# Kernel optimization log

Hardware: AMD Instinct MI355X
Metric: run time of the kernel (lower is better)

Reference implementation:

```python
import jax, jax.numpy as jnp
import numpy as np
from jax import lax

SOS_IDX = 1
EOS_IDX = 2

B, T, K = 32, 256, 128


def setup_inputs() -> dict:
    key = jax.random.key(0)
    k1, k2, k3, k4 = jax.random.split(key, 4)
    h = jax.random.normal(k1, (B, T, K), dtype=jnp.float32)
    transition = jax.random.normal(k2, (K, K), dtype=jnp.float32) * 0.1
    y = jax.random.randint(k3, (B, T), 0, K)
    lengths = jnp.maximum(jax.random.randint(k4, (B,), 1, T + 1), 1)
    mask = jnp.arange(T)[None, :] < lengths[:, None]  # [B, T] bool, contiguous prefix
    return {"h": h, "transition": transition, "y": y, "lengths": lengths, "mask": mask}


def reference(h, transition, y, lengths, mask):
    """CRF negative log-likelihood, same math as CRF.nll."""
    b, t_len, k = h.shape
    # crf_scores[b,t,i,j] = h[b,t,j] + transition[i,j]
    scores = h[:, :, None, :] + transition[None, None, :, :]  # [B,T,K,K]

    # Golden path score: score of transition prev_tag -> tag at each valid step.
    prev_y = jnp.concatenate(
        [jnp.full((b, 1), SOS_IDX, dtype=y.dtype), y[:, :-1]], axis=1
    )  # [B,T]
    gold = jnp.take_along_axis(
        jnp.take_along_axis(scores, prev_y[:, :, None, None], axis=2)[:, :, 0, :],
        y[:, :, None],
        axis=2,
    )[:, :, 0]  # [B,T]
    golden_scores = jnp.sum(jnp.where(mask, gold, jnp.zeros((), h.dtype)))

    # Forward (alpha) recurrence in log space; freeze alpha past sequence end.
    alpha0 = scores[:, 0, SOS_IDX, :]  # [B,K] (all lengths >= 1)
    scores_tbkk = jnp.swapaxes(scores, 0, 1)  # [T,B,K,K]
    mask_tb = jnp.swapaxes(mask, 0, 1)  # [T,B]

    def step(alpha, xs):
        s_t, m_t = xs  # [B,K,K], [B]
        new_alpha = jax.nn.logsumexp(s_t + alpha[:, :, None], axis=1)  # [B,K]
        return jnp.where(m_t[:, None], new_alpha, alpha), None

    alpha, _ = lax.scan(step, alpha0, (scores_tbkk[1:], mask_tb[1:]))
    Z = jnp.sum(alpha[:, EOS_IDX])
    loss = (Z - golden_scores) / b
    return loss
```

## Files before the change

kernel.cpp:

```cpp
#include <hip/hip_runtime.h>
#include <stdint.h>

#define SOS_IDX 1
#define EOS_IDX 2
#define Bb 32
#define Tt 256
#define Kk 128
#define SK 136
#define CSP 16

typedef unsigned short ushort_t;
typedef __attribute__((ext_vector_type(8))) short short8;
typedef __attribute__((ext_vector_type(4))) float float4v;

__device__ __forceinline__ ushort_t f2bf(float x) {
    union { float f; uint32_t u; } c; c.f = x;
    uint32_t u = c.u + 0x7FFFu + ((c.u >> 16) & 1u);
    return (ushort_t)(u >> 16);
}
__device__ __forceinline__ float bf2f(ushort_t s) {
    union { uint32_t u; float f; } c; c.u = ((uint32_t)s) << 16;
    return c.f;
}
__device__ __forceinline__ float bflo(uint32_t u) {
    union { uint32_t u; float f; } c; c.u = u << 16; return c.f;
}
__device__ __forceinline__ float bfhi(uint32_t u) {
    union { uint32_t u; float f; } c; c.u = u & 0xFFFF0000u; return c.f;
}
__device__ __forceinline__ uint32_t pk2bf(float a, float b) {
    union { float f; uint32_t u; } ca, cb; ca.f = a; cb.f = b;
    uint32_t ua = ca.u + 0x7FFFu + ((ca.u >> 16) & 1u);
    uint32_t ub = cb.u + 0x7FFFu + ((cb.u >> 16) & 1u);
    return __builtin_amdgcn_perm(ub, ua, 0x07060302u);
}

__global__ __launch_bounds__(256) void crf_prep(const float* __restrict__ trans,
                                                ushort_t* __restrict__ ETT,
                                                ushort_t* __restrict__ ET) {
    const int tid = threadIdx.x, bid = blockIdx.x;
    int idx = ((bid & 7) * 256 + tid) * 8;
    if (bid < 8) {
        int m = idx >> 7, k0 = idx & 127;
        float e[8];
#pragma unroll
        for (int r = 0; r < 8; ++r) e[r] = __expf(trans[(k0 + r) * Kk + m]);
        uint4 o;
        o.x = pk2bf(e[0], e[1]); o.y = pk2bf(e[2], e[3]);
        o.z = pk2bf(e[4], e[5]); o.w = pk2bf(e[6], e[7]);
        *(uint4*)&ETT[idx] = o;
    } else {
        float4 a = *(const float4*)&trans[idx];
        float4 b = *(const float4*)&trans[idx + 4];
        uint4 o;
        o.x = pk2bf(__expf(a.x), __expf(a.y));
        o.y = pk2bf(__expf(a.z), __expf(a.w));
        o.z = pk2bf(__expf(b.x), __expf(b.y));
        o.w = pk2bf(__expf(b.z), __expf(b.w));
        *(uint4*)&ET[idx] = o;
    }
}

__global__ __launch_bounds__(128, 2) void crf_stageA(const float* __restrict__ h,
                                                     const ushort_t* __restrict__ ETT,
                                                     const ushort_t* __restrict__ ET,
                                                     const int* __restrict__ lengths,
                                                     ushort_t* __restrict__ Qt,
                                                     float* __restrict__ Ls,
                                                     int NC) {
    const int st = blockIdx.x, b = blockIdx.y, c = blockIdx.z;
    const int tid = threadIdx.x;
    const int lane = tid & 63, w = tid >> 6;
    const int c15 = lane & 15, q = lane >> 4;
    const int len = lengths[b];
    int ts = c * CSP; if (ts < 1) ts = 1;
    int te = (c + 1) * CSP; if (te > Tt) te = Tt;
    const int tE = te < len ? te : len;
    if (ts >= tE) return;
    const int nsteps = tE - ts;
    const size_t qoff = ((size_t)b * NC + c) * (Kk * Kk);
    const int nbase = st * 32;

    __shared__ __align__(16) ushort_t s_S[2][32 * SK];
    __shared__ __align__(16) float    s_eh[CSP][Kk];
    __shared__ float s_wmax[2][2];

    for (int tl = w; tl < nsteps; tl += 2) {
        const float* hr = &h[((size_t)b * Tt + ts + tl) * Kk];
        s_eh[tl][lane]      = __expf(hr[lane]);
        s_eh[tl][lane + 64] = __expf(hr[lane + 64]);
    }

    short8 afr[4][4];
#pragma unroll
    for (int mt = 0; mt < 4; ++mt)
#pragma unroll
        for (int kt = 0; kt < 4; ++kt)
            afr[mt][kt] = *(const short8*)&ETT[(w * 64 + mt * 16 + c15) * Kk + kt * 32 + q * 8];
    __syncthreads();

    {
        float lmax = 0.0f;
#pragma unroll
        for (int j = 0; j < 4; ++j) {
            int idx = j * 128 + tid;
            int nl = idx >> 4, k8 = (idx & 15) * 8;
            uint4 ev = *(const uint4*)&ET[(nbase + nl) * Kk + k8];
            float4 e0 = *(const float4*)&s_eh[0][k8];
            float4 e1 = *(const float4*)&s_eh[0][k8 + 4];
            float v0 = bflo(ev.x) * e0.x, v1 = bfhi(ev.x) * e0.y;
            float v2 = bflo(ev.y) * e0.z, v3 = bfhi(ev.y) * e0.w;
            float v4 = bflo(ev.z) * e1.x, v5 = bfhi(ev.z) * e1.y;
            float v6 = bflo(ev.w) * e1.z, v7 = bfhi(ev.w) * e1.w;
            lmax = fmaxf(lmax, fmaxf(fmaxf(fmaxf(v0, v1), fmaxf(v2, v3)),
                                     fmaxf(fmaxf(v4, v5), fmaxf(v6, v7))));
            uint4 o;
            o.x = pk2bf(v0, v1); o.y = pk2bf(v2, v3);
            o.z = pk2bf(v4, v5); o.w = pk2bf(v6, v7);
            *(uint4*)&s_S[0][nl * SK + k8] = o;
        }
#pragma unroll
        for (int o = 1; o < 64; o <<= 1) lmax = fmaxf(lmax, __shfl_xor(lmax, o));
        if (lane == 0) s_wmax[0][w] = lmax;
    }
    __syncthreads();

    float L = 0.0f;
    int cur = 0;
    for (int s = 1; s < nsteps; ++s) {
        float invG = 1.0f;
        if ((s & 3) == 0) {
            int ms = ((s >> 2) - 1) & 1;
            float g = fmaxf(s_wmax[ms][0], s_wmax[ms][1]);
            invG = 1.0f / g;
            L += __logf(g);
        }
        const bool isMark = ((s & 3) == 3) || (s == nsteps - 1);

        float sc[4][4];
#pragma unroll
        for (int mt = 0; mt < 4; ++mt) {
            float4 e = *(const float4*)&s_eh[s][w * 64 + mt * 16 + q * 4];
            sc[mt][0] = e.x * invG; sc[mt][1] = e.y * invG;
            sc[mt][2] = e.z * invG; sc[mt][3] = e.w * invG;
        }

        short8 bfr[2][4];
        const ushort_t* ps = s_S[cur];
#pragma unroll
        for (int nt = 0; nt < 2; ++nt)
#pragma unroll
            for (int kt = 0; kt < 4; ++kt)
                bfr[nt][kt] = *(const short8*)&ps[(nt * 16 + c15) * SK + kt * 32 + q * 8];

        float4v acc[4][2];
#pragma unroll
        for (int mt = 0; mt < 4; ++mt)
#pragma unroll
            for (int nt = 0; nt < 2; ++nt) acc[mt][nt] = (float4v){0.f, 0.f, 0.f, 0.f};
#pragma unroll
        for (int kt = 0; kt < 4; ++kt)
#pragma unroll
            for (int mt = 0; mt < 4; ++mt)
#pragma unroll
                for (int nt = 0; nt < 2; ++nt)
                    acc[mt][nt] = __builtin_amdgcn_mfma_f32_16x16x32_bf16(
                        afr[mt][kt], bfr[nt][kt], acc[mt][nt], 0, 0, 0);

        int nxt = cur ^ 1;
        ushort_t* pn = s_S[nxt];
        float lmax = 0.0f;
#pragma unroll
        for (int mt = 0; mt < 4; ++mt)
#pragma unroll
            for (int nt = 0; nt < 2; ++nt) {
                float v0 = acc[mt][nt][0] * sc[mt][0];
                float v1 = acc[mt][nt][1] * sc[mt][1];
                float v2 = acc[mt][nt][2] * sc[mt][2];
                float v3 = acc[mt][nt][3] * sc[mt][3];
                if (isMark)
                    lmax = fmaxf(lmax, fmaxf(fmaxf(v0, v1), fmaxf(v2, v3)));
                uint2 u; u.x = pk2bf(v0, v1); u.y = pk2bf(v2, v3);
                *(uint2*)&pn[(nt * 16 + c15) * SK + w * 64 + mt * 16 + q * 4] = u;
            }
        if (isMark) {
#pragma unroll
            for (int o = 1; o < 64; o <<= 1) lmax = fmaxf(lmax, __shfl_xor(lmax, o));
            if (lane == 0) s_wmax[(s >> 2) & 1][w] = lmax;
        }
        __syncthreads();
        cur = nxt;
    }

    int fs = ((nsteps - 1) >> 2) & 1;
    float Gf = fmaxf(s_wmax[fs][0], s_wmax[fs][1]);
    float dsc = 1.0f / Gf;
    L += __logf(Gf);
    const ushort_t* pc = s_S[cur];
#pragma unroll
    for (int j = 0; j < 4; ++j) {
        int idx = j * 128 + tid;
        int n = idx & 127, o = idx >> 7;
        uint4 gv; ushort_t* gp = (ushort_t*)&gv;
#pragma unroll
        for (int r = 0; r < 8; ++r)
            gp[r] = f2bf(bf2f(pc[(o * 8 + r) * SK + n]) * dsc);
        *(uint4*)&Qt[qoff + (size_t)n * Kk + nbase + o * 8] = gv;
    }
    if (tid == 0) Ls[(((size_t)b * NC + c) << 2) + st] = L;
}

__global__ __launch_bounds__(512, 1) void crf_stageB(const float* __restrict__ h,
                                                     const float* __restrict__ trans,
                                                     const int* __restrict__ y,
                                                     const int* __restrict__ lengths,
                                                     const ushort_t* __restrict__ Qt,
                                                     const float* __restrict__ Ls,
                                                     float* __restrict__ out,
                                                     int NC) {
    const int b = blockIdx.x;
    const int tid = threadIdx.x;
    const int lane = tid & 63, w = tid >> 6;
    const int n = tid >> 2, qr = tid & 3;
    const int len = lengths[b];

    __shared__ __align__(16) float vbuf[2][Kk];
    __shared__ float s_wmax[2][8];
    __shared__ float red[8];
    __shared__ float gred[4];

    if (w < 4) {
        float g = 0.0f;
        if (tid < len) {
            int yt   = y[b * Tt + tid];
            int prev = (tid == 0) ? SOS_IDX : y[b * Tt + tid - 1];
            g = h[((size_t)b * Tt + tid) * Kk + yt] + trans[prev * Kk + yt];
        }
#pragma unroll
        for (int off = 32; off > 0; off >>= 1) g += __shfl_down(g, off);
        if (lane == 0) gred[w] = g;
    }

    float a0 = h[((size_t)b * Tt) * Kk + n] + trans[SOS_IDX * Kk + n];
    float m0 = a0;
#pragma unroll
    for (int o = 1; o < 64; o <<= 1) m0 = fmaxf(m0, __shfl_xor(m0, o));
    if (lane == 0) red[w] = m0;
    __syncthreads();
    {
        float4 r0 = *(const float4*)&red[0];
        float4 r1 = *(const float4*)&red[4];
        m0 = fmaxf(fmaxf(fmaxf(r0.x, r0.y), fmaxf(r0.z, r0.w)),
                   fmaxf(fmaxf(r1.x, r1.y), fmaxf(r1.z, r1.w)));
    }
    float cacc = m0;
    if (qr == 0) vbuf[0][n] = __expf(a0 - m0);

    const int NCR = (len <= 1) ? 0 : min(NC, (len + CSP - 1) / CSP);
    const size_t lbase = (size_t)b * NC;
    uint4 qb[4];
    if (NCR > 0) {
        const uint4* qp = (const uint4*)(Qt + lbase * (Kk * Kk) + n * Kk + qr * 32);
#pragma unroll
        for (int r = 0; r < 4; ++r) qb[r] = qp[r];
    }
    __syncthreads();
    if (tid == 0)
        atomicAdd(out, -(gred[0] + gred[1] + gred[2] + gred[3]) * (1.0f / (float)Bb));

    int cur = 0;
    for (int ci = 0; ci < NCR; ++ci) {
        uint4 qn[4];
        if (ci + 1 < NCR) {
            const uint4* qp2 = (const uint4*)(Qt + (lbase + ci + 1) * (Kk * Kk) + n * Kk + qr * 32);
#pragma unroll
            for (int r = 0; r < 4; ++r) qn[r] = qp2[r];
        }
        float4 Ls4 = *(const float4*)&Ls[(lbase + ci) << 2];
        float Lref = fmaxf(fmaxf(Ls4.x, Ls4.y), fmaxf(Ls4.z, Ls4.w));
        float lsq = (qr == 0) ? Ls4.x : (qr == 1) ? Ls4.y : (qr == 2) ? Ls4.z : Ls4.w;
        float eQ = __expf(lsq - Lref);
        float invG = 1.0f;
        if (ci > 0 && (ci & 3) == 0) {
            int ms = ((ci >> 2) - 1) & 1;
            float4 r0 = *(const float4*)&s_wmax[ms][0];
            float4 r1 = *(const float4*)&s_wmax[ms][4];
            float g = fmaxf(fmaxf(fmaxf(r0.x, r0.y), fmaxf(r0.z, r0.w)),
                            fmaxf(fmaxf(r1.x, r1.y), fmaxf(r1.z, r1.w)));
            invG = 1.0f / g;
            cacc += __logf(g);
        }
        cacc += Lref;

        float acc0 = 0.0f, acc1 = 0.0f;
#pragma unroll
        for (int r = 0; r < 4; ++r) {
            uint4 d = qb[r];
            float4 v0 = *(const float4*)&vbuf[cur][qr * 32 + r * 8];
            float4 v1 = *(const float4*)&vbuf[cur][qr * 32 + r * 8 + 4];
            acc0 = fmaf(bflo(d.x), v0.x, acc0);
            acc1 = fmaf(bfhi(d.x), v0.y, acc1);
            acc0 = fmaf(bflo(d.y), v0.z, acc0);
            acc1 = fmaf(bfhi(d.y), v0.w, acc1);
            acc0 = fmaf(bflo(d.z), v1.x, acc0);
            acc1 = fmaf(bfhi(d.z), v1.y, acc1);
            acc0 = fmaf(bflo(d.w), v1.z, acc0);
            acc1 = fmaf(bfhi(d.w), v1.w, acc1);
        }
        float s = (acc0 + acc1) * (eQ * invG);
        s += __shfl_xor(s, 1);
        s += __shfl_xor(s, 2);

        const bool isMark = ((ci & 3) == 3) || (ci == NCR - 1);
        if (isMark) {
            float wm = s;
#pragma unroll
            for (int o = 1; o < 64; o <<= 1) wm = fmaxf(wm, __shfl_xor(wm, o));
            if (lane == 0) s_wmax[(ci >> 2) & 1][w] = wm;
        }
        int nxt = cur ^ 1;
        if (qr == 0) vbuf[nxt][n] = s;
        __syncthreads();
        cur = nxt;
        if (ci + 1 < NCR) {
#pragma unroll
            for (int r = 0; r < 4; ++r) qb[r] = qn[r];
        }
    }

    if (tid == 0) {
        atomicAdd(out, (cacc + __logf(vbuf[cur][EOS_IDX])) * (1.0f / (float)Bb));
    }
}

extern "C" void kernel_launch(void* const* d_in, const int* in_sizes, int n_in,
                              void* d_out, int out_size, void* d_ws, size_t ws_size,
                              hipStream_t stream) {
    const float* h       = (const float*)d_in[0];
    const float* trans   = (const float*)d_in[1];
    const int*   y       = (const int*)d_in[2];
    const int*   lengths = (const int*)d_in[3];
    float* out = (float*)d_out;

    const int NC = Tt / CSP;
    ushort_t* Qt  = (ushort_t*)d_ws;
    ushort_t* ETT = Qt + (size_t)Bb * NC * Kk * Kk;
    ushort_t* ET  = ETT + Kk * Kk;
    float*    Ls  = (float*)(ET + Kk * Kk);

    hipMemsetAsync(out, 0, sizeof(float), stream);
    crf_prep<<<16, 256, 0, stream>>>(trans, ETT, ET);
    crf_stageA<<<dim3(4, Bb, NC), 128, 0, stream>>>(h, ETT, ET, lengths, Qt, Ls, NC);
    crf_stageB<<<Bb, 512, 0, stream>>>(h, trans, y, lengths, Qt, Ls, out, NC);
}
```

Baseline: 112.8 us.

## Fuse prep, chunk-product and combine stages into one kernel with last-block combine

Merges the three kernels into one. Each block now computes exp(transition) to bf16 directly instead of reading a precomputed table. The per-batch serial combine runs in whichever block finishes last, detected with an atomic counter per batch and threadfences. This removes two launches and the launch gaps between stages, but adds redundant exp work in every block, an extra memset, and a serial combine done by only 128 threads with no prefetch of the next Qt chunk.

```diff
diff --git a/kernel.cpp b/kernel.cpp
--- a/kernel.cpp
+++ b/kernel.cpp
@@ -8,6 +8,7 @@
 #define Kk 128
 #define SK 136
 #define CSP 16
+#define NCc 16
 
 typedef unsigned short ushort_t;
 typedef __attribute__((ext_vector_type(8))) short short8;
@@ -35,55 +36,44 @@
     return __builtin_amdgcn_perm(ub, ua, 0x07060302u);
 }
 
-__global__ __launch_bounds__(256) void crf_prep(const float* __restrict__ trans,
-                                                ushort_t* __restrict__ ETT,
-                                                ushort_t* __restrict__ ET) {
-    const int tid = threadIdx.x, bid = blockIdx.x;
-    int idx = ((bid & 7) * 256 + tid) * 8;
-    if (bid < 8) {
-        int m = idx >> 7, k0 = idx & 127;
-        float e[8];
-#pragma unroll
-        for (int r = 0; r < 8; ++r) e[r] = __expf(trans[(k0 + r) * Kk + m]);
-        uint4 o;
-        o.x = pk2bf(e[0], e[1]); o.y = pk2bf(e[2], e[3]);
-        o.z = pk2bf(e[4], e[5]); o.w = pk2bf(e[6], e[7]);
-        *(uint4*)&ETT[idx] = o;
-    } else {
-        float4 a = *(const float4*)&trans[idx];
-        float4 b = *(const float4*)&trans[idx + 4];
-        uint4 o;
-        o.x = pk2bf(__expf(a.x), __expf(a.y));
-        o.y = pk2bf(__expf(a.z), __expf(a.w));
-        o.z = pk2bf(__expf(b.x), __expf(b.y));
-        o.w = pk2bf(__expf(b.z), __expf(b.w));
-        *(uint4*)&ET[idx] = o;
-    }
-}
-
-__global__ __launch_bounds__(128, 2) void crf_stageA(const float* __restrict__ h,
-                                                     const ushort_t* __restrict__ ETT,
-                                                     const ushort_t* __restrict__ ET,
-                                                     const int* __restrict__ lengths,
-                                                     ushort_t* __restrict__ Qt,
-                                                     float* __restrict__ Ls,
-                                                     int NC) {
+__global__ __launch_bounds__(128, 2) void crf_fused(const float* __restrict__ h,
+                                                    const float* __restrict__ trans,
+                                                    const int* __restrict__ y,
+                                                    const int* __restrict__ lengths,
+                                                    ushort_t* __restrict__ Qt,
+                                                    float* __restrict__ Ls,
+                                                    unsigned* __restrict__ cnt,
+                                                    float* __restrict__ out) {
     const int st = blockIdx.x, b = blockIdx.y, c = blockIdx.z;
     const int tid = threadIdx.x;
     const int lane = tid & 63, w = tid >> 6;
     const int c15 = lane & 15, q = lane >> 4;
     const int len = lengths[b];
+    const int NCRb = (len <= 1) ? 0 : ((len + CSP - 1) / CSP);
     int ts = c * CSP; if (ts < 1) ts = 1;
     int te = (c + 1) * CSP; if (te > Tt) te = Tt;
     const int tE = te < len ? te : len;
-    if (ts >= tE) return;
-    const int nsteps = tE - ts;
-    const size_t qoff = ((size_t)b * NC + c) * (Kk * Kk);
-    const int nbase = st * 32;
 
     __shared__ __align__(16) ushort_t s_S[2][32 * SK];
     __shared__ __align__(16) float    s_eh[CSP][Kk];
     __shared__ float s_wmax[2][2];
+    __shared__ __align__(16) float vbuf[2][Kk];
+    __shared__ float s_wm[2][2];
+    __shared__ float red2[2], gred2[2];
+    __shared__ unsigned s_last;
+
+    if (ts >= tE) {
+        if (st == 0 && c == 0 && tid == 0) {
+            int y0 = y[b * Tt];
+            float gold0 = h[(size_t)b * Tt * Kk + y0] + trans[SOS_IDX * Kk + y0];
+            float zb = h[(size_t)b * Tt * Kk + EOS_IDX] + trans[SOS_IDX * Kk + EOS_IDX];
+            atomicAdd(out, (zb - gold0) * (1.0f / (float)Bb));
+        }
+        return;
+    }
+    const int nsteps = tE - ts;
+    const size_t qoff = ((size_t)b * NCc + c) * (Kk * Kk);
+    const int nbase = st * 32;
 
     for (int tl = w; tl < nsteps; tl += 2) {
         const float* hr = &h[((size_t)b * Tt + ts + tl) * Kk];
@@ -95,8 +85,16 @@
 #pragma unroll
     for (int mt = 0; mt < 4; ++mt)
 #pragma unroll
-        for (int kt = 0; kt < 4; ++kt)
-            afr[mt][kt] = *(const short8*)&ETT[(w * 64 + mt * 16 + c15) * Kk + kt * 32 + q * 8];
+        for (int kt = 0; kt < 4; ++kt) {
+            short8 f;
+            int m = w * 64 + mt * 16 + c15;
+#pragma unroll
+            for (int j = 0; j < 8; ++j) {
+                int k = kt * 32 + q * 8 + j;
+                f[j] = (short)f2bf(__expf(trans[k * Kk + m]));
+            }
+            afr[mt][kt] = f;
+        }
     __syncthreads();
 
     {
@@ -105,13 +103,13 @@
         for (int j = 0; j < 4; ++j) {
             int idx = j * 128 + tid;
             int nl = idx >> 4, k8 = (idx & 15) * 8;
-            uint4 ev = *(const uint4*)&ET[(nbase + nl) * Kk + k8];
+            const float* tr = &trans[(nbase + nl) * Kk + k8];
             float4 e0 = *(const float4*)&s_eh[0][k8];
             float4 e1 = *(const float4*)&s_eh[0][k8 + 4];
-            float v0 = bflo(ev.x) * e0.x, v1 = bfhi(ev.x) * e0.y;
-            float v2 = bflo(ev.y) * e0.z, v3 = bfhi(ev.y) * e0.w;
-            float v4 = bflo(ev.z) * e1.x, v5 = bfhi(ev.z) * e1.y;
-            float v6 = bflo(ev.w) * e1.z, v7 = bfhi(ev.w) * e1.w;
+            float v0 = __expf(tr[0]) * e0.x, v1 = __expf(tr[1]) * e0.y;
+            float v2 = __expf(tr[2]) * e0.z, v3 = __expf(tr[3]) * e0.w;
+            float v4 = __expf(tr[4]) * e1.x, v5 = __expf(tr[5]) * e1.y;
+            float v6 = __expf(tr[6]) * e1.z, v7 = __expf(tr[7]) * e1.w;
             lmax = fmaxf(lmax, fmaxf(fmaxf(fmaxf(v0, v1), fmaxf(v2, v3)),
                                      fmaxf(fmaxf(v4, v5), fmaxf(v6, v7))));
             uint4 o;
@@ -207,129 +205,100 @@
             gp[r] = f2bf(bf2f(pc[(o * 8 + r) * SK + n]) * dsc);
         *(uint4*)&Qt[qoff + (size_t)n * Kk + nbase + o * 8] = gv;
     }
-    if (tid == 0) Ls[(((size_t)b * NC + c) << 2) + st] = L;
-}
-
-__global__ __launch_bounds__(512, 1) void crf_stageB(const float* __restrict__ h,
-                                                     const float* __restrict__ trans,
-                                                     const int* __restrict__ y,
-                                                     const int* __restrict__ lengths,
-                                                     const ushort_t* __restrict__ Qt,
-                                                     const float* __restrict__ Ls,
-                                                     float* __restrict__ out,
-                                                     int NC) {
-    const int b = blockIdx.x;
-    const int tid = threadIdx.x;
-    const int lane = tid & 63, w = tid >> 6;
-    const int n = tid >> 2, qr = tid & 3;
-    const int len = lengths[b];
-
-    __shared__ __align__(16) float vbuf[2][Kk];
-    __shared__ float s_wmax[2][8];
-    __shared__ float red[8];
-    __shared__ float gred[4];
-
-    if (w < 4) {
+    if (tid == 0) Ls[(((size_t)b * NCc + c) << 2) + st] = L;
+
+    __threadfence();
+    __syncthreads();
+    if (tid == 0) {
+        unsigned old = atomicAdd(&cnt[b], 1u);
+        s_last = (old == (unsigned)(4 * NCRb) - 1u) ? 1u : 0u;
+    }
+    __syncthreads();
+    if (!s_last) return;
+    __threadfence();
+
+    {
         float g = 0.0f;
         if (tid < len) {
             int yt   = y[b * Tt + tid];
             int prev = (tid == 0) ? SOS_IDX : y[b * Tt + tid - 1];
             g = h[((size_t)b * Tt + tid) * Kk + yt] + trans[prev * Kk + yt];
         }
+        int t1 = tid + 128;
+        if (t1 < len) {
+            int yt   = y[b * Tt + t1];
+            int prev = y[b * Tt + t1 - 1];
+            g += h[((size_t)b * Tt + t1) * Kk + yt] + trans[prev * Kk + yt];
+        }
 #pragma unroll
         for (int off = 32; off > 0; off >>= 1) g += __shfl_down(g, off);
-        if (lane == 0) gred[w] = g;
-    }
-
-    float a0 = h[((size_t)b * Tt) * Kk + n] + trans[SOS_IDX * Kk + n];
+        if (lane == 0) gred2[w] = g;
+    }
+
+    float a0 = h[((size_t)b * Tt) * Kk + tid] + trans[SOS_IDX * Kk + tid];
     float m0 = a0;
 #pragma unroll
     for (int o = 1; o < 64; o <<= 1) m0 = fmaxf(m0, __shfl_xor(m0, o));
-    if (lane == 0) red[w] = m0;
-    __syncthreads();
-    {
-        float4 r0 = *(const float4*)&red[0];
-        float4 r1 = *(const float4*)&red[4];
-        m0 = fmaxf(fmaxf(fmaxf(r0.x, r0.y), fmaxf(r0.z, r0.w)),
-                   fmaxf(fmaxf(r1.x, r1.y), fmaxf(r1.z, r1.w)));
-    }
+    if (lane == 0) red2[w] = m0;
+    __syncthreads();
+    m0 = fmaxf(red2[0], red2[1]);
     float cacc = m0;
-    if (qr == 0) vbuf[0][n] = __expf(a0 - m0);
-
-    const int NCR = (len <= 1) ? 0 : min(NC, (len + CSP - 1) / CSP);
-    const size_t lbase = (size_t)b * NC;
-    uint4 qb[4];
-    if (NCR > 0) {
-        const uint4* qp = (const uint4*)(Qt + lbase * (Kk * Kk) + n * Kk + qr * 32);
-#pragma unroll
-        for (int r = 0; r < 4; ++r) qb[r] = qp[r];
-    }
-    __syncthreads();
-    if (tid == 0)
-        atomicAdd(out, -(gred[0] + gred[1] + gred[2] + gred[3]) * (1.0f / (float)Bb));
-
-    int cur = 0;
-    for (int ci = 0; ci < NCR; ++ci) {
-        uint4 qn[4];
-        if (ci + 1 < NCR) {
-            const uint4* qp2 = (const uint4*)(Qt + (lbase + ci + 1) * (Kk * Kk) + n * Kk + qr * 32);
-#pragma unroll
-            for (int r = 0; r < 4; ++r) qn[r] = qp2[r];
-        }
+    vbuf[0][tid] = __expf(a0 - m0);
+    __syncthreads();
+
+    const size_t lbase = (size_t)b * NCc;
+    int cb = 0;
+    for (int ci = 0; ci < NCRb; ++ci) {
         float4 Ls4 = *(const float4*)&Ls[(lbase + ci) << 2];
         float Lref = fmaxf(fmaxf(Ls4.x, Ls4.y), fmaxf(Ls4.z, Ls4.w));
-        float lsq = (qr == 0) ? Ls4.x : (qr == 1) ? Ls4.y : (qr == 2) ? Ls4.z : Ls4.w;
-        float eQ = __expf(lsq - Lref);
+        float e0 = __expf(Ls4.x - Lref), e1 = __expf(Ls4.y - Lref);
+        float e2 = __expf(Ls4.z - Lref), e3 = __expf(Ls4.w - Lref);
         float invG = 1.0f;
         if (ci > 0 && (ci & 3) == 0) {
             int ms = ((ci >> 2) - 1) & 1;
-            float4 r0 = *(const float4*)&s_wmax[ms][0];
-            float4 r1 = *(const float4*)&s_wmax[ms][4];
-            float g = fmaxf(fmaxf(fmaxf(r0.x, r0.y), fmaxf(r0.z, r0.w)),
-                            fmaxf(fmaxf(r1.x, r1.y), fmaxf(r1.z, r1.w)));
-            invG = 1.0f / g;
-            cacc += __logf(g);
+            float gg = fmaxf(s_wm[ms][0], s_wm[ms][1]);
+            invG = 1.0f / gg;
+            cacc += __logf(gg);
         }
         cacc += Lref;
 
-        float acc0 = 0.0f, acc1 = 0.0f;
-#pragma unroll
-        for (int r = 0; r < 4; ++r) {
-            uint4 d = qb[r];
-            float4 v0 = *(const float4*)&vbuf[cur][qr * 32 + r * 8];
-            float4 v1 = *(const float4*)&vbuf[cur][qr * 32 + r * 8 + 4];
-            acc0 = fmaf(bflo(d.x), v0.x, acc0);
-            acc1 = fmaf(bfhi(d.x), v0.y, acc1);
-            acc0 = fmaf(bflo(d.y), v0.z, acc0);
-            acc1 = fmaf(bfhi(d.y), v0.w, acc1);
-            acc0 = fmaf(bflo(d.z), v1.x, acc0);
-            acc1 = fmaf(bfhi(d.z), v1.y, acc1);
-            acc0 = fmaf(bflo(d.w), v1.z, acc0);
-            acc1 = fmaf(bfhi(d.w), v1.w, acc1);
-        }
-        float s = (acc0 + acc1) * (eQ * invG);
-        s += __shfl_xor(s, 1);
-        s += __shfl_xor(s, 2);
-
-        const bool isMark = ((ci & 3) == 3) || (ci == NCR - 1);
+        const uint4* qp = (const uint4*)(Qt + (lbase + ci) * (Kk * Kk) + (size_t)tid * Kk);
+        float p0 = 0.f, p1 = 0.f, p2 = 0.f, p3 = 0.f;
+#pragma unroll
+        for (int r = 0; r < 16; ++r) {
+            uint4 d = qp[r];
+            float4 v0 = *(const float4*)&vbuf[cb][r * 8];
+            float4 v1 = *(const float4*)&vbuf[cb][r * 8 + 4];
+            float* pp = (r < 4) ? &p0 : (r < 8) ? &p1 : (r < 12) ? &p2 : &p3;
+            float a = *pp;
+            a = fmaf(bflo(d.x), v0.x, a);
+            a = fmaf(bfhi(d.x), v0.y, a);
+            a = fmaf(bflo(d.y), v0.z, a);
+            a = fmaf(bfhi(d.y), v0.w, a);
+            a = fmaf(bflo(d.z), v1.x, a);
+            a = fmaf(bfhi(d.z), v1.y, a);
+            a = fmaf(bflo(d.w), v1.z, a);
+            a = fmaf(bfhi(d.w), v1.w, a);
+            *pp = a;
+        }
+        float s = (fmaf(e0, p0, e1 * p1) + fmaf(e2, p2, e3 * p3)) * invG;
+
+        const bool isMark = ((ci & 3) == 3) || (ci == NCRb - 1);
         if (isMark) {
             float wm = s;
 #pragma unroll
             for (int o = 1; o < 64; o <<= 1) wm = fmaxf(wm, __shfl_xor(wm, o));
-            if (lane == 0) s_wmax[(ci >> 2) & 1][w] = wm;
-        }
-        int nxt = cur ^ 1;
-        if (qr == 0) vbuf[nxt][n] = s;
+            if (lane == 0) s_wm[(ci >> 2) & 1][w] = wm;
+        }
+        int nxt = cb ^ 1;
+        vbuf[nxt][tid] = s;
         __syncthreads();
-        cur = nxt;
-        if (ci + 1 < NCR) {
-#pragma unroll
-            for (int r = 0; r < 4; ++r) qb[r] = qn[r];
-        }
+        cb = nxt;
     }
 
     if (tid == 0) {
-        atomicAdd(out, (cacc + __logf(vbuf[cur][EOS_IDX])) * (1.0f / (float)Bb));
+        float zb = cacc + __logf(vbuf[cb][EOS_IDX]);
+        atomicAdd(out, (zb - (gred2[0] + gred2[1])) * (1.0f / (float)Bb));
     }
 }
 
@@ -342,14 +311,11 @@
     const int*   lengths = (const int*)d_in[3];
     float* out = (float*)d_out;
 
-    const int NC = Tt / CSP;
     ushort_t* Qt  = (ushort_t*)d_ws;
-    ushort_t* ETT = Qt + (size_t)Bb * NC * Kk * Kk;
-    ushort_t* ET  = ETT + Kk * Kk;
-    float*    Ls  = (float*)(ET + Kk * Kk);
+    float*    Ls  = (float*)(Qt + (size_t)Bb * NCc * Kk * Kk);
+    unsigned* cnt = (unsigned*)(Ls + (size_t)Bb * NCc * 4);
 
     hipMemsetAsync(out, 0, sizeof(float), stream);
-    crf_prep<<<16, 256, 0, stream>>>(trans, ETT, ET);
-    crf_stageA<<<dim3(4, Bb, NC), 128, 0, stream>>>(h, ETT, ET, lengths, Qt, Ls, NC);
-    crf_stageB<<<Bb, 512, 0, stream>>>(h, trans, y, lengths, Qt, Ls, out, NC);
-}
+    hipMemsetAsync(Ls, 0, (size_t)Bb * NCc * 4 * sizeof(float) + Bb * sizeof(unsigned), stream);
+    crf_fused<<<dim3(4, Bb, NCc), 128, 0, stream>>>(h, trans, y, lengths, Qt, Ls, cnt, out);
+}
```

Result: slower. 188.3 us (+66.9%).
